# Kernel tuning notes

Hardware: AMD Instinct MI355X
Metric: run time of the kernel (lower is better)

The kernel has to match this reference:

```python
import jax, jax.numpy as jnp
import numpy as np

MEM_SIZE = 100000
EMB = 1024
HEADS = 8
HEAD_DIM = EMB // HEADS
TOPK = 10
BATCH = 2048


def setup_inputs() -> dict:
    key = jax.random.key(0)
    ks = jax.random.split(key, 10)
    query = jax.random.normal(ks[0], (BATCH, EMB), dtype=jnp.float32)
    memory = jax.random.normal(ks[1], (MEM_SIZE, EMB), dtype=jnp.float32) * 0.1
    s = 1.0 / np.sqrt(EMB)
    w_q = jax.random.normal(ks[2], (EMB, EMB), dtype=jnp.float32) * s
    w_k = jax.random.normal(ks[3], (EMB, EMB), dtype=jnp.float32) * s
    w_v = jax.random.normal(ks[4], (EMB, EMB), dtype=jnp.float32) * s
    b_q = jnp.zeros((EMB,), jnp.float32)
    b_k = jnp.zeros((EMB,), jnp.float32)
    b_v = jnp.zeros((EMB,), jnp.float32)
    w_o = jax.random.normal(ks[5], (EMB, EMB), dtype=jnp.float32) * s
    b_o = jnp.zeros((EMB,), jnp.float32)
    return {"query": query, "memory": memory, "w_q": w_q, "w_k": w_k,
            "w_v": w_v, "b_q": b_q, "b_k": b_k, "b_v": b_v,
            "w_o": w_o, "b_o": b_o}


def reference(query, memory, w_q, w_k, w_v, b_q, b_k, b_v, w_o, b_o):
    B = query.shape[0]
    # similarity + top-k retrieval: [B, M] -> indices [B, K]
    sim = jnp.matmul(query, memory.T)
    _, idx = jax.lax.top_k(sim, TOPK)
    mem_sel = memory[idx]                       # [B, K, E] gather
    # MultiheadAttention: query is one token, keys/values = retrieved memories
    q = (query @ w_q.T + b_q).reshape(B, HEADS, HEAD_DIM)
    k = (mem_sel @ w_k.T + b_k).reshape(B, TOPK, HEADS, HEAD_DIM)
    v = (mem_sel @ w_v.T + b_v).reshape(B, TOPK, HEADS, HEAD_DIM)
    scale = 1.0 / np.sqrt(HEAD_DIM)
    scores = jnp.einsum('bhd,bkhd->bhk', q, k) * scale   # [B, H, K]
    attn = jax.nn.softmax(scores, axis=-1)
    ctx = jnp.einsum('bhk,bkhd->bhd', attn, v).reshape(B, EMB)
    return ctx @ w_o.T + b_o
```

## Files before the change

kernel.cpp:

```cpp
#include <hip/hip_runtime.h>
#include <cstdint>
#include <cstddef>

#define BATCH   2048
#define EMB     1024
#define HEADS   8
#define HDIM    128
#define TOPK    10
#define MEMN    100000
#define NTILES  782
#define CHUNKS  64
#define TPC     13
#define CAND    20
#define SCALE   0.08838834764831845f

typedef _Float16 h16;
typedef _Float16 half8 __attribute__((ext_vector_type(8)));
typedef _Float16 half4 __attribute__((ext_vector_type(4)));
typedef float    f32x4 __attribute__((ext_vector_type(4)));

__device__ __forceinline__ void gl_lds16(const void* g, void* l) {
  __builtin_amdgcn_global_load_lds(
      (const __attribute__((address_space(1))) unsigned int*)g,
      (__attribute__((address_space(3))) unsigned int*)l, 16, 0, 0);
}

__device__ __forceinline__ void bar_sync() {
  asm volatile("" ::: "memory");
  __builtin_amdgcn_s_barrier();
  __builtin_amdgcn_sched_barrier(0);
}
__device__ __forceinline__ void bar_wait6() {
  asm volatile("s_waitcnt vmcnt(6)" ::: "memory");
  __builtin_amdgcn_s_barrier();
  __builtin_amdgcn_sched_barrier(0);
}
__device__ __forceinline__ void bar_wait0() {
  asm volatile("s_waitcnt vmcnt(0)" ::: "memory");
  __builtin_amdgcn_s_barrier();
  __builtin_amdgcn_sched_barrier(0);
}

template <int N>
__device__ __forceinline__ void topk_ins(float (&tv)[N], int (&ti)[N],
                                         float s, int gi) {
  float cv = s; int ci = gi;
#pragma unroll
  for (int j = 0; j < N; ++j) {
    bool sw = tv[j] < cv;
    float tf = tv[j]; int tt = ti[j];
    if (sw) { tv[j] = cv; ti[j] = ci; cv = tf; ci = tt; }
  }
}

__global__ void __launch_bounds__(256) k_f2h(
    const float* __restrict__ in, h16* __restrict__ out, long n4)
{
  long i = (long)blockIdx.x * 256 + threadIdx.x;
  const long stride = (long)gridDim.x * 256;
  for (; i < n4; i += stride) {
    const f32x4 v = ((const f32x4*)in)[i];
    half4 o;
#pragma unroll
    for (int j = 0; j < 4; ++j) o[j] = (h16)v[j];
    ((half4*)out)[i] = o;
  }
}

__global__ void __launch_bounds__(256) k_f2hT(
    const float* __restrict__ in, h16* __restrict__ out)
{
  __shared__ float tl[64][65];
  const int n0 = blockIdx.x * 64, e0 = blockIdx.y * 64;
  const int cc = threadIdx.x & 63, rb = threadIdx.x >> 6;
#pragma unroll
  for (int i = 0; i < 16; ++i) {
    const int r = i * 4 + rb;
    tl[r][cc] = in[(size_t)(n0 + r) * EMB + e0 + cc];
  }
  __syncthreads();
#pragma unroll
  for (int i = 0; i < 16; ++i) {
    const int r = i * 4 + rb;
    out[(size_t)(e0 + r) * EMB + n0 + cc] = (h16)tl[cc][r];
  }
}

__device__ __forceinline__ void sim_stage2(
    const h16* __restrict__ query, const h16* __restrict__ memory,
    char* smem, int buf, int r0, int n0, int k0, int w, int l)
{
  h16* dA = (h16*)(smem + buf * 32768);
  h16* dB = (h16*)(smem + 65536 + buf * 16384);
#pragma unroll
  for (int i = 0; i < 4; ++i) {
    const int ch = i * 512 + w * 64 + l;
    const int row = ch >> 3;
    const int kc = (ch & 7) ^ (row & 7);
    gl_lds16(query + (size_t)(r0 + row) * EMB + k0 + kc * 8,
             dA + (size_t)(i * 512 + w * 64) * 8);
  }
#pragma unroll
  for (int i = 0; i < 2; ++i) {
    const int ch = i * 512 + w * 64 + l;
    const int row = ch >> 3;
    const int kc = (ch & 7) ^ (row & 7);
    int n = n0 + row; if (n > MEMN - 1) n = MEMN - 1;
    gl_lds16(memory + (size_t)n * EMB + k0 + kc * 8,
             dB + (size_t)(i * 512 + w * 64) * 8);
  }
}

__device__ __forceinline__ void sim_comp2(
    const char* smem, int buf, int wr, int wc, int l, f32x4 (&acc)[4][4])
{
  const h16* sA = (const h16*)(smem + buf * 32768);
  const h16* sB = (const h16*)(smem + 65536 + buf * 16384);
#pragma unroll
  for (int ks = 0; ks < 2; ++ks) {
    half8 af[4], bfr[4];
#pragma unroll
    for (int mi = 0; mi < 4; ++mi) {
      const int row = wr * 64 + mi * 16 + (l & 15);
      const int slot = (ks * 4 + (l >> 4)) ^ (row & 7);
      af[mi] = *(const half8*)&sA[row * 64 + slot * 8];
    }
#pragma unroll
    for (int ni = 0; ni < 4; ++ni) {
      const int row = wc * 64 + ni * 16 + (l & 15);
      const int slot = (ks * 4 + (l >> 4)) ^ (row & 7);
      bfr[ni] = *(const half8*)&sB[row * 64 + slot * 8];
    }
    __builtin_amdgcn_s_setprio(1);
#pragma unroll
    for (int mi = 0; mi < 4; ++mi)
#pragma unroll
      for (int ni = 0; ni < 4; ++ni)
        acc[mi][ni] = __builtin_amdgcn_mfma_f32_16x16x32_f16(
            af[mi], bfr[ni], acc[mi][ni], 0, 0, 0);
    __builtin_amdgcn_s_setprio(0);
  }
}

__global__ void __launch_bounds__(512) k_sim_h(
    const h16* __restrict__ query, const h16* __restrict__ memory,
    float* __restrict__ cand_val, int* __restrict__ cand_idx)
{
  const int c  = blockIdx.y;
  const int r0 = blockIdx.x * 256;
  __shared__ __align__(16) char smem[98304];
  float* lS = (float*)smem;

  const int t = threadIdx.x, w = t >> 6, l = t & 63;
  const int wr = w >> 1, wc = w & 1;
  const int row_s = t >> 2, qq = t & 3;

  float tvA[TOPK], tvB[TOPK]; int tiA[TOPK], tiB[TOPK];
#pragma unroll
  for (int j = 0; j < TOPK; ++j) { tvA[j] = -3.0e38f; tvB[j] = -3.0e38f; tiA[j] = 0; tiB[j] = 0; }

  const int tile_beg = c * TPC;
  int tile_end = tile_beg + TPC; if (tile_end > NTILES) tile_end = NTILES;

  for (int tile = tile_beg; tile < tile_end; ++tile) {
    const int n0 = tile * 128;
    f32x4 acc[4][4] = {};

    sim_stage2(query, memory, smem, 0, r0, n0, 0, w, l);
#pragma unroll 1
    for (int kt = 0; kt < 14; kt += 2) {
      sim_stage2(query, memory, smem, 1, r0, n0, (kt + 1) * 64, w, l);
      bar_wait6();
      sim_comp2(smem, 0, wr, wc, l, acc);
      bar_sync();
      sim_stage2(query, memory, smem, 0, r0, n0, (kt + 2) * 64, w, l);
      bar_wait6();
      sim_comp2(smem, 1, wr, wc, l, acc);
      bar_sync();
    }
    sim_stage2(query, memory, smem, 1, r0, n0, 15 * 64, w, l);
    bar_wait6();
    sim_comp2(smem, 0, wr, wc, l, acc);
    bar_sync();
    bar_wait0();
    sim_comp2(smem, 1, wr, wc, l, acc);
    __syncthreads();

#pragma unroll
    for (int ph = 0; ph < 2; ++ph) {
      if ((wr >> 1) == ph) {
#pragma unroll
        for (int mi = 0; mi < 4; ++mi)
#pragma unroll
          for (int ni = 0; ni < 4; ++ni)
#pragma unroll
            for (int r = 0; r < 4; ++r) {
              const int row_l = (wr & 1) * 64 + mi * 16 + (l >> 4) * 4 + r;
              const int col = wc * 64 + ni * 16 + (l & 15);
              lS[row_l * 132 + col] = acc[mi][ni][r];
            }
      }
      __syncthreads();
      float (&tv)[TOPK] = ph ? tvB : tvA; int (&ti)[TOPK] = ph ? tiB : tiA;
#pragma unroll
      for (int cc = 0; cc < 8; ++cc) {
        const int c4 = qq * 32 + ((cc + qq * 2) & 7) * 4;
        const f32x4 v = *(const f32x4*)&lS[row_s * 132 + c4];
        const float m = fmaxf(fmaxf(v[0], v[1]), fmaxf(v[2], v[3]));
        if (m > tv[TOPK - 1]) {
#pragma unroll
          for (int j = 0; j < 4; ++j) {
            const int g = n0 + c4 + j;
            if (g < MEMN && v[j] > tv[TOPK - 1]) topk_ins<TOPK>(tv, ti, v[j], g);
          }
        }
      }
      __syncthreads();
    }
  }

  float* lSv = (float*)smem;
  int*   lSi = (int*)(smem + 20480);
#pragma unroll
  for (int ph = 0; ph < 2; ++ph) {
#pragma unroll
    for (int j = 0; j < TOPK; ++j) {
      lSv[row_s * 40 + qq * TOPK + j] = ph ? tvB[j] : tvA[j];
      lSi[row_s * 40 + qq * TOPK + j] = ph ? tiB[j] : tiA[j];
    }
    __syncthreads();
    if (qq == 0) {
      float fv[TOPK]; int fi[TOPK];
#pragma unroll
      for (int j = 0; j < TOPK; ++j) { fv[j] = -3.0e38f; fi[j] = 0; }
      for (int m = 0; m < 40; ++m) {
        const float s = lSv[row_s * 40 + m];
        if (s > fv[TOPK - 1]) topk_ins<TOPK>(fv, fi, s, lSi[row_s * 40 + m]);
      }
      const int grow = r0 + ph * 128 + row_s;
#pragma unroll
      for (int j = 0; j < TOPK; ++j) {
        cand_val[(size_t)(c * TOPK + j) * BATCH + grow] = fv[j];
        cand_idx[(size_t)(c * TOPK + j) * BATCH + grow] = fi[j];
      }
    }
    __syncthreads();
  }
}

__global__ void __launch_bounds__(256) k_sim_f32(
    const float* __restrict__ query, const float* __restrict__ memory,
    float* __restrict__ cand_val, int* __restrict__ cand_idx)
{
  const int c  = blockIdx.x;
  const int r0 = blockIdx.y * 128;
  __shared__ __align__(16) char smem[65536];
  float* lA = (float*)smem;
  float* lB = (float*)(smem + 32768);
  float* lS = (float*)smem;

  const int t = threadIdx.x, w = t >> 6, l = t & 63;
  const int wr = w >> 1, wc = w & 1;
  const int row_s = t >> 2, qq = t & 3;

  float tvA[TOPK], tvB[TOPK]; int tiA[TOPK], tiB[TOPK];
#pragma unroll
  for (int j = 0; j < TOPK; ++j) { tvA[j] = -3.0e38f; tvB[j] = -3.0e38f; tiA[j] = 0; tiB[j] = 0; }

  const int tile_beg = c * TPC;
  int tile_end = tile_beg + TPC; if (tile_end > NTILES) tile_end = NTILES;

  for (int tile = tile_beg; tile < tile_end; ++tile) {
    const int n0 = tile * 128;
    f32x4 acc[4][4] = {};

    for (int kt = 0; kt < 16; ++kt) {
      const int k0 = kt * 64;
#pragma unroll
      for (int i = 0; i < 8; ++i) {
        const int c16 = (w * 8 + i) * 64 + l;
        const int row = c16 >> 4, s16 = c16 & 15;
        const int src = s16 ^ (row & 7);
        gl_lds16(query + (size_t)(r0 + row) * EMB + k0 + src * 4,
                 lA + (size_t)(w * 8 + i) * 256);
        int n = n0 + row; if (n > MEMN - 1) n = MEMN - 1;
        gl_lds16(memory + (size_t)n * EMB + k0 + src * 4,
                 lB + (size_t)(w * 8 + i) * 256);
      }
      __syncthreads();
#pragma unroll
      for (int ks = 0; ks < 2; ++ks) {
        half8 af[4], bfr[4];
#pragma unroll
        for (int mi = 0; mi < 4; ++mi) {
          const int row = wr * 64 + mi * 16 + (l & 15);
          const int g = ks * 4 + (l >> 4), m7 = row & 7;
          const f32x4 a0 = *(const f32x4*)(lA + row * 64 + (((2 * g)     ^ m7) << 2));
          const f32x4 a1 = *(const f32x4*)(lA + row * 64 + (((2 * g + 1) ^ m7) << 2));
          half8 f;
#pragma unroll
          for (int j = 0; j < 4; ++j) { f[j] = (h16)a0[j]; f[4 + j] = (h16)a1[j]; }
          af[mi] = f;
        }
#pragma unroll
        for (int ni = 0; ni < 4; ++ni) {
          const int row = wc * 64 + ni * 16 + (l & 15);
          const int g = ks * 4 + (l >> 4), m7 = row & 7;
          const f32x4 b0 = *(const f32x4*)(lB + row * 64 + (((2 * g)     ^ m7) << 2));
          const f32x4 b1 = *(const f32x4*)(lB + row * 64 + (((2 * g + 1) ^ m7) << 2));
          half8 f;
#pragma unroll
          for (int j = 0; j < 4; ++j) { f[j] = (h16)b0[j]; f[4 + j] = (h16)b1[j]; }
          bfr[ni] = f;
        }
#pragma unroll
        for (int mi = 0; mi < 4; ++mi)
#pragma unroll
          for (int ni = 0; ni < 4; ++ni)
            acc[mi][ni] = __builtin_amdgcn_mfma_f32_16x16x32_f16(
                af[mi], bfr[ni], acc[mi][ni], 0, 0, 0);
      }
      __syncthreads();
    }

#pragma unroll
    for (int ph = 0; ph < 2; ++ph) {
      if (wr == ph) {
#pragma unroll
        for (int mi = 0; mi < 4; ++mi)
#pragma unroll
          for (int ni = 0; ni < 4; ++ni)
#pragma unroll
            for (int r = 0; r < 4; ++r) {
              const int row_l = mi * 16 + (l >> 4) * 4 + r;
              const int col = wc * 64 + ni * 16 + (l & 15);
              lS[row_l * 131 + col] = acc[mi][ni][r];
            }
      }
      __syncthreads();
      float (&tv)[TOPK] = ph ? tvB : tvA; int (&ti)[TOPK] = ph ? tiB : tiA;
#pragma unroll 8
      for (int cc = 0; cc < 32; ++cc) {
        const int colt = qq * 32 + ((cc + qq * 8) & 31);
        const float s = lS[row_s * 131 + colt];
        const int g = n0 + colt;
        if (g < MEMN && s > tv[TOPK - 1]) topk_ins<TOPK>(tv, ti, s, g);
      }
      __syncthreads();
    }
  }

  float* lSv = (float*)smem;
  int*   lSi = (int*)(smem + 10240);
#pragma unroll
  for (int ph = 0; ph < 2; ++ph) {
#pragma unroll
    for (int j = 0; j < TOPK; ++j) {
      lSv[row_s * 40 + qq * TOPK + j] = ph ? tvB[j] : tvA[j];
      lSi[row_s * 40 + qq * TOPK + j] = ph ? tiB[j] : tiA[j];
    }
    __syncthreads();
    if (qq == 0) {
      float fv[TOPK]; int fi[TOPK];
#pragma unroll
      for (int j = 0; j < TOPK; ++j) { fv[j] = -3.0e38f; fi[j] = 0; }
      for (int m = 0; m < 40; ++m) {
        const float s = lSv[row_s * 40 + m];
        if (s > fv[TOPK - 1]) topk_ins<TOPK>(fv, fi, s, lSi[row_s * 40 + m]);
      }
      const int grow = r0 + ph * 64 + row_s;
#pragma unroll
      for (int j = 0; j < TOPK; ++j) {
        cand_val[(size_t)(c * TOPK + j) * BATCH + grow] = fv[j];
        cand_idx[(size_t)(c * TOPK + j) * BATCH + grow] = fi[j];
      }
    }
    __syncthreads();
  }
}

__global__ void __launch_bounds__(256) k_merge20(
    const float* __restrict__ cand_val, const int* __restrict__ cand_idx,
    int* __restrict__ idx20, int nch)
{
  const int row = blockIdx.x * 256 + threadIdx.x;
  float tv[CAND]; int ti[CAND];
#pragma unroll
  for (int j = 0; j < CAND; ++j) { tv[j] = -3.0e38f; ti[j] = 0; }
  for (int m = 0; m < nch * TOPK; ++m) {
    const float s = cand_val[(size_t)m * BATCH + row];
    if (s > tv[CAND - 1]) {
      const int gi = cand_idx[(size_t)m * BATCH + row];
      topk_ins<CAND>(tv, ti, s, gi);
    }
  }
#pragma unroll
  for (int j = 0; j < CAND; ++j) idx20[row * CAND + j] = ti[j];
}

__global__ void __launch_bounds__(256) k_rescore(
    const float* __restrict__ query, const float* __restrict__ memory,
    const int* __restrict__ idx20, int* __restrict__ idx10)
{
  const int w = threadIdx.x >> 6, l = threadIdx.x & 63;
  const int b = blockIdx.x * 4 + w;
  const float* qp = query + (size_t)b * EMB + l * 16;
  float q[16];
#pragma unroll
  for (int j = 0; j < 4; ++j) {
    const f32x4 v = *(const f32x4*)(qp + 4 * j);
#pragma unroll
    for (int i = 0; i < 4; ++i) q[j * 4 + i] = v[i];
  }
  double sc[CAND];
#pragma unroll
  for (int cc = 0; cc < CAND; ++cc) {
    const int mi = idx20[b * CAND + cc];
    const float* mp = memory + (size_t)mi * EMB + l * 16;
    double s = 0.0;
#pragma unroll
    for (int j = 0; j < 4; ++j) {
      const f32x4 v = *(const f32x4*)(mp + 4 * j);
#pragma unroll
      for (int i = 0; i < 4; ++i) s += (double)q[j * 4 + i] * (double)v[i];
    }
#pragma unroll
    for (int o = 1; o < 64; o <<= 1) s += __shfl_xor(s, o);
    sc[cc] = s;
  }
  if (l == 0) {
    unsigned used = 0;
#pragma unroll
    for (int j = 0; j < TOPK; ++j) {
      double best = -1.0e300; int bi = 0;
#pragma unroll
      for (int cc = 0; cc < CAND; ++cc)
        if (!((used >> cc) & 1u) && sc[cc] > best) { best = sc[cc]; bi = cc; }
      used |= 1u << bi;
      idx10[b * TOPK + j] = idx20[b * CAND + bi];
    }
  }
}

__global__ void __launch_bounds__(256) k_gemm16(
    const h16* __restrict__ A, int astr, int acol, int aoffz,
    const h16* __restrict__ Bt, int bcol, int boffz,
    const float* __restrict__ bias, int biasoffz,
    h16* __restrict__ outH, float* __restrict__ outF,
    int cstr, int ccol, int coffz, int nkt)
{
  const int z = blockIdx.z;
  acol += z * aoffz; bcol += z * boffz; ccol += z * coffz;
  const float* bp = bias ? bias + z * biasoffz : nullptr;

  const int c0 = blockIdx.x * 128, r0 = blockIdx.y * 128;
  __shared__ __align__(16) h16 lA[128 * 64], lB[128 * 64];
  const int t = threadIdx.x, w = t >> 6, l = t & 63;
  const int wr = w >> 1, wc = w & 1;
  f32x4 acc[4][4] = {};

  for (int kt = 0; kt < nkt; ++kt) {
    const int k0 = kt * 64;
#pragma unroll
    for (int i = 0; i < 4; ++i) {
      const int ch = w * 256 + i * 64 + l;
      const int row = ch >> 3;
      const int kc = (ch & 7) ^ (row & 7);
      gl_lds16(A  + (size_t)(r0 + row) * astr + acol + k0 + kc * 8,
               lA + (size_t)(w * 256 + i * 64) * 8);
      gl_lds16(Bt + (size_t)(c0 + row) * EMB + bcol + k0 + kc * 8,
               lB + (size_t)(w * 256 + i * 64) * 8);
    }
    __syncthreads();
#pragma unroll
    for (int ks = 0; ks < 2; ++ks) {
      half8 af[4], bfr[4];
#pragma unroll
      for (int mi = 0; mi < 4; ++mi) {
        const int row = wr * 64 + mi * 16 + (l & 15);
        const int slot = (ks * 4 + (l >> 4)) ^ (row & 7);
        af[mi] = *(const half8*)&lA[row * 64 + slot * 8];
      }
#pragma unroll
      for (int ni = 0; ni < 4; ++ni) {
        const int row = wc * 64 + ni * 16 + (l & 15);
        const int slot = (ks * 4 + (l >> 4)) ^ (row & 7);
        bfr[ni] = *(const half8*)&lB[row * 64 + slot * 8];
      }
#pragma unroll
      for (int mi = 0; mi < 4; ++mi)
#pragma unroll
        for (int ni = 0; ni < 4; ++ni)
          acc[mi][ni] = __builtin_amdgcn_mfma_f32_16x16x32_f16(
              af[mi], bfr[ni], acc[mi][ni], 0, 0, 0);
    }
    __syncthreads();
  }
#pragma unroll
  for (int ni = 0; ni < 4; ++ni) {
    const int ncol = c0 + wc * 64 + ni * 16 + (l & 15);
    const float bv = bp ? bp[ncol] : 0.0f;
#pragma unroll
    for (int mi = 0; mi < 4; ++mi)
#pragma unroll
      for (int r = 0; r < 4; ++r) {
        const int grow = r0 + wr * 64 + mi * 16 + (l >> 4) * 4 + r;
        const float v = acc[mi][ni][r] + bv;
        if (outH) outH[(size_t)grow * cstr + ccol + ncol] = (h16)v;
        else      outF[(size_t)grow * cstr + ccol + ncol] = v;
      }
  }
}

__global__ void __launch_bounds__(256) k_attn(
    const float* __restrict__ memory, const int* __restrict__ idx10,
    h16* __restrict__ qtA)
{
  const int w = threadIdx.x >> 6, l = threadIdx.x & 63;
  const int b = blockIdx.x * 4 + w;
  int rows[TOPK];
#pragma unroll
  for (int k = 0; k < TOPK; ++k) rows[k] = idx10[b * TOPK + k];

  for (int h = 0; h < HEADS; ++h) {
    h16* qp = qtA + (size_t)b * (HEADS * EMB) + h * EMB + l * 16;
    const half8 qa = *(const half8*)qp;
    const half8 qb = *(const half8*)(qp + 8);
    float qf[16];
#pragma unroll
    for (int j = 0; j < 8; ++j) { qf[j] = (float)qa[j]; qf[8 + j] = (float)qb[j]; }

    float sc[TOPK];
#pragma unroll
    for (int k = 0; k < TOPK; ++k) {
      const float* mp = memory + (size_t)rows[k] * EMB + l * 16;
      float p = 0.f;
#pragma unroll
      for (int j = 0; j < 4; ++j) {
        const f32x4 m = *(const f32x4*)(mp + 4 * j);
#pragma unroll
        for (int i = 0; i < 4; ++i) p += qf[j * 4 + i] * m[i];
      }
#pragma unroll
      for (int o = 1; o < 64; o <<= 1) p += __shfl_xor(p, o);
      sc[k] = p * SCALE;
    }
    float mx = sc[0];
#pragma unroll
    for (int k = 1; k < TOPK; ++k) mx = fmaxf(mx, sc[k]);
    float e[TOPK], den = 0.f;
#pragma unroll
    for (int k = 0; k < TOPK; ++k) { e[k] = __expf(sc[k] - mx); den += e[k]; }
    const float inv = 1.0f / den;

    float acc[16];
#pragma unroll
    for (int j = 0; j < 16; ++j) acc[j] = 0.f;
#pragma unroll
    for (int k = 0; k < TOPK; ++k) {
      const float* mp = memory + (size_t)rows[k] * EMB + l * 16;
#pragma unroll
      for (int j = 0; j < 4; ++j) {
        const f32x4 m = *(const f32x4*)(mp + 4 * j);
#pragma unroll
        for (int i = 0; i < 4; ++i) acc[j * 4 + i] += e[k] * m[i];
      }
    }
    half8 o0, o1;
#pragma unroll
    for (int j = 0; j < 8; ++j) {
      o0[j] = (h16)(acc[j] * inv);
      o1[j] = (h16)(acc[8 + j] * inv);
    }
    *(half8*)qp = o0;
    *(half8*)(qp + 8) = o1;
  }
}

extern "C" void kernel_launch(void* const* d_in, const int* in_sizes, int n_in,
                              void* d_out, int out_size, void* d_ws, size_t ws_size,
                              hipStream_t stream)
{
  const float* query  = (const float*)d_in[0];
  const float* memory = (const float*)d_in[1];
  const float* w_q    = (const float*)d_in[2];
  const float* w_k    = (const float*)d_in[3];
  const float* w_v    = (const float*)d_in[4];
  const float* b_q    = (const float*)d_in[5];
  const float* b_v    = (const float*)d_in[7];
  const float* w_o    = (const float*)d_in[8];
  const float* b_o    = (const float*)d_in[9];

  char* ws = (char*)d_ws;
  float* cand_val = (float*)(ws + 0);
  int*   cand_idx = (int*)  (ws + 5242880);
  int*   idx20    = (int*)  (ws + 10485760);
  int*   idx10    = (int*)  (ws + 10649600);
  h16*   qH       = (h16*)  (ws + 10731520);
  h16*   wqH      = (h16*)  (ws + 14925824);
  h16*   wkTH     = (h16*)  (ws + 17022976);
  h16*   wvH      = (h16*)  (ws + 19120128);
  h16*   woH      = (h16*)  (ws + 21217280);
  h16*   qpH      = (h16*)  (ws + 23314432);
  h16*   qtA      = (h16*)  (ws + 27508736);
  h16*   ctxH     = (h16*)  (ws + 61063168);
  h16*   memH     = (h16*)  (ws + 65257472);

  const bool fast = ws_size >= 270057472ULL;

  if (fast) k_f2h<<<8192, 256, 0, stream>>>(memory, memH, 25600000L);
  k_f2h <<<2048, 256, 0, stream>>>(query, qH, 524288L);
  k_f2h <<<1024, 256, 0, stream>>>(w_q, wqH, 262144L);
  k_f2hT<<<dim3(16, 16), 256, 0, stream>>>(w_k, wkTH);
  k_f2h <<<1024, 256, 0, stream>>>(w_v, wvH, 262144L);
  k_f2h <<<1024, 256, 0, stream>>>(w_o, woH, 262144L);

  if (fast) k_sim_h  <<<dim3(8, CHUNKS), 512, 0, stream>>>(qH, memH, cand_val, cand_idx);
  else      k_sim_f32<<<dim3(CHUNKS, 16), 256, 0, stream>>>(query, memory, cand_val, cand_idx);
  k_merge20<<<BATCH / 256, 256, 0, stream>>>(cand_val, cand_idx, idx20, CHUNKS);
  k_rescore<<<BATCH / 4, 256, 0, stream>>>(query, memory, idx20, idx10);

  k_gemm16<<<dim3(8, 16), 256, 0, stream>>>(qH, EMB, 0, 0, wqH, 0, 0,
                                            b_q, 0, qpH, nullptr, EMB, 0, 0, 16);
  k_gemm16<<<dim3(8, 16, 8), 256, 0, stream>>>(qpH, EMB, 0, HDIM, wkTH, 0, HDIM,
                                               nullptr, 0, qtA, nullptr,
                                               HEADS * EMB, 0, EMB, 2);
  k_attn<<<BATCH / 4, 256, 0, stream>>>(memory, idx10, qtA);
  k_gemm16<<<dim3(1, 16, 8), 256, 0, stream>>>(qtA, HEADS * EMB, 0, EMB,
                                               wvH, 0, HDIM * EMB,
                                               b_v, HDIM, ctxH, nullptr,
                                               EMB, 0, HDIM, 16);
  k_gemm16<<<dim3(8, 16), 256, 0, stream>>>(ctxH, EMB, 0, 0, woH, 0, 0,
                                            b_o, 0, nullptr, (float*)d_out,
                                            EMB, 0, 0, 16);
}
```

Baseline: 2.532 ms.

## Deepen memory-tile prefetch to four LDS buffers in similarity GEMM

Splits the staging of query and memory tiles so the memory (B) operand is prefetched two k-steps ahead through four LDS buffers, while the query (A) operand stays double-buffered. The k-loop is fully unrolled with waitcnt levels adjusted per step. The goal is to hide more global-load latency on the streamed memory matrix. In exchange LDS use per block rises from 96KB to 128KB, which may cut occupancy, and code size grows.

```diff
diff --git a/kernel.cpp b/kernel.cpp
--- a/kernel.cpp
+++ b/kernel.cpp
@@ -14,6 +14,7 @@
 #define CAND    20
 #define SCALE   0.08838834764831845f
 
+
 typedef _Float16 h16;
 typedef _Float16 half8 __attribute__((ext_vector_type(8)));
 typedef _Float16 half4 __attribute__((ext_vector_type(4)));
@@ -32,6 +33,11 @@
 }
 __device__ __forceinline__ void bar_wait6() {
   asm volatile("s_waitcnt vmcnt(6)" ::: "memory");
+  __builtin_amdgcn_s_barrier();
+  __builtin_amdgcn_sched_barrier(0);
+}
+__device__ __forceinline__ void bar_wait4() {
+  asm volatile("s_waitcnt vmcnt(4)" ::: "memory");
   __builtin_amdgcn_s_barrier();
   __builtin_amdgcn_sched_barrier(0);
 }
@@ -86,12 +92,11 @@
   }
 }
 
-__device__ __forceinline__ void sim_stage2(
-    const h16* __restrict__ query, const h16* __restrict__ memory,
-    char* smem, int buf, int r0, int n0, int k0, int w, int l)
+__device__ __forceinline__ void sim_stageA(
+    const h16* __restrict__ query, char* smem, int buf,
+    int r0, int k0, int w, int l)
 {
   h16* dA = (h16*)(smem + buf * 32768);
-  h16* dB = (h16*)(smem + 65536 + buf * 16384);
 #pragma unroll
   for (int i = 0; i < 4; ++i) {
     const int ch = i * 512 + w * 64 + l;
@@ -100,6 +105,13 @@
     gl_lds16(query + (size_t)(r0 + row) * EMB + k0 + kc * 8,
              dA + (size_t)(i * 512 + w * 64) * 8);
   }
+}
+
+__device__ __forceinline__ void sim_stageB(
+    const h16* __restrict__ memory, char* smem, int buf,
+    int n0, int k0, int w, int l)
+{
+  h16* dB = (h16*)(smem + 65536 + buf * 16384);
 #pragma unroll
   for (int i = 0; i < 2; ++i) {
     const int ch = i * 512 + w * 64 + l;
@@ -112,10 +124,11 @@
 }
 
 __device__ __forceinline__ void sim_comp2(
-    const char* smem, int buf, int wr, int wc, int l, f32x4 (&acc)[4][4])
-{
-  const h16* sA = (const h16*)(smem + buf * 32768);
-  const h16* sB = (const h16*)(smem + 65536 + buf * 16384);
+    const char* smem, int abuf, int bbuf, int wr, int wc, int l,
+    f32x4 (&acc)[4][4])
+{
+  const h16* sA = (const h16*)(smem + abuf * 32768);
+  const h16* sB = (const h16*)(smem + 65536 + bbuf * 16384);
 #pragma unroll
   for (int ks = 0; ks < 2; ++ks) {
     half8 af[4], bfr[4];
@@ -148,7 +161,7 @@
 {
   const int c  = blockIdx.y;
   const int r0 = blockIdx.x * 256;
-  __shared__ __align__(16) char smem[98304];
+  __shared__ __align__(16) char smem[131072];
   float* lS = (float*)smem;
 
   const int t = threadIdx.x, w = t >> 6, l = t & 63;
@@ -166,25 +179,20 @@
     const int n0 = tile * 128;
     f32x4 acc[4][4] = {};
 
-    sim_stage2(query, memory, smem, 0, r0, n0, 0, w, l);
-#pragma unroll 1
-    for (int kt = 0; kt < 14; kt += 2) {
-      sim_stage2(query, memory, smem, 1, r0, n0, (kt + 1) * 64, w, l);
-      bar_wait6();
-      sim_comp2(smem, 0, wr, wc, l, acc);
+    sim_stageB(memory, smem, 0, n0, 0,   w, l);
+    sim_stageB(memory, smem, 1, n0, 64,  w, l);
+    sim_stageA(query,  smem, 0, r0, 0,   w, l);
+
+#pragma unroll
+    for (int i = 0; i < 16; ++i) {
+      if (i < 14) sim_stageB(memory, smem, (i + 2) & 3, n0, (i + 2) * 64, w, l);
+      if (i < 15) sim_stageA(query,  smem, (i + 1) & 1, r0, (i + 1) * 64, w, l);
+      if (i <= 13)      bar_wait6();
+      else if (i == 14) bar_wait4();
+      else              bar_wait0();
+      sim_comp2(smem, i & 1, i & 3, wr, wc, l, acc);
       bar_sync();
-      sim_stage2(query, memory, smem, 0, r0, n0, (kt + 2) * 64, w, l);
-      bar_wait6();
-      sim_comp2(smem, 1, wr, wc, l, acc);
-      bar_sync();
-    }
-    sim_stage2(query, memory, smem, 1, r0, n0, 15 * 64, w, l);
-    bar_wait6();
-    sim_comp2(smem, 0, wr, wc, l, acc);
-    bar_sync();
-    bar_wait0();
-    sim_comp2(smem, 1, wr, wc, l, acc);
-    __syncthreads();
+    }
 
 #pragma unroll
     for (int ph = 0; ph < 2; ++ph) {
@@ -598,7 +606,7 @@
   int*   idx10    = (int*)  (ws + 10649600);
   h16*   qH       = (h16*)  (ws + 10731520);
   h16*   wqH      = (h16*)  (ws + 14925824);
-  h16*   wkTH     = (h16*)  (ws + 17022976);
+  h16*   wkTH    = (h16*)  (ws + 17022976);
   h16*   wvH      = (h16*)  (ws + 19120128);
   h16*   woH      = (h16*)  (ws + 21217280);
   h16*   qpH      = (h16*)  (ws + 23314432);
```

Result: slower. 2.889 ms (+14.1%).
